# Kernel optimization log

Measured on AMD Instinct MI355X. Metric: run time of the kernel, lower is better.

The kernel has to match this reference:

```python
import jax, jax.numpy as jnp
import numpy as np
from jax import lax

B, C, T, K, L, G = 4, 256, 2048, 7, 2, 32


def _conv1d(x, w, b, pad=0, groups=1):
    # x: [B,C,T], w: [O, C//groups, kw]
    y = lax.conv_general_dilated(x, w, window_strides=(1,), padding=[(pad, pad)],
                                 dimension_numbers=("NCH", "OIH", "NCH"),
                                 feature_group_count=groups)
    return y + b[None, :, None]


def _conv2d(x, w, b, pad=(0, 0), groups=1):
    # x: [B,C,H,W], w: [O, C//groups, kh, kw]
    y = lax.conv_general_dilated(x, w, window_strides=(1, 1),
                                 padding=[(pad[0], pad[0]), (pad[1], pad[1])],
                                 dimension_numbers=("NCHW", "OIHW", "NCHW"),
                                 feature_group_count=groups)
    return y + b[None, :, None, None]


def _knn_dis(x, k):
    # x: [B,C,T] -> neighbor indices [B,T,k] by (negative) squared euclidean distance
    xx = jnp.sum(x * x, axis=1)                       # [B,T]
    inner = jnp.einsum("bcm,bcn->bmn", x, x)          # [B,T,T]
    pd = -xx[:, :, None] + 2.0 * inner - xx[:, None, :]  # -||x_m - x_n||^2
    _, idx = lax.top_k(pd, k)                          # nearest = largest of -dist^2
    return idx


def _graph_feature(x, idx):
    # x: [B,C,T], idx: [B,T,K] -> style=1 feature [B,2C,T,K] = cat(neighbor, center)
    xt = jnp.transpose(x, (0, 2, 1))                   # [B,T,C]
    bidx = jnp.arange(x.shape[0])[:, None, None]
    nb = xt[bidx, idx]                                 # [B,T,K,C] gather
    ctr = jnp.broadcast_to(xt[:, :, None, :], nb.shape)
    feat = jnp.concatenate([nb, ctr], axis=-1)         # [B,T,K,2C]
    return jnp.transpose(feat, (0, 3, 1, 2))           # [B,2C,T,K]


def setup_inputs() -> dict:
    key = jax.random.key(0)
    ks = jax.random.split(key, 9)
    s = 0.05
    return {
        "x": jax.random.normal(ks[0], (B, C, T), jnp.float32),
        "tw1": jax.random.normal(ks[1], (L, C, C, 1), jnp.float32) * s,
        "tb1": jax.random.normal(ks[2], (L, C), jnp.float32) * s,
        "tw2": jax.random.normal(ks[3], (L, C, C // G, 5), jnp.float32) * s,
        "tb2": jax.random.normal(ks[4], (L, C), jnp.float32) * s,
        "dw1": jax.random.normal(ks[5], (L, C, 2 * C, 1, 1), jnp.float32) * s,
        "db1": jax.random.normal(ks[6], (L, C), jnp.float32) * s,
        "dw2": jax.random.normal(ks[7], (L, C, C // G, 5, 5), jnp.float32) * s,
        "db2": jax.random.normal(ks[8], (L, C), jnp.float32) * s,
    }


def reference(x, tw1, tb1, tw2, tb2, dw1, db1, dw2, db2):
    for i in range(L):
        identity = x
        # temporal branch: 1x1 conv -> GELU -> grouped conv1d k=5 (pad=2)
        h = jax.nn.gelu(_conv1d(x, tw1[i], tb1[i]), approximate=False)
        tout = _conv1d(h, tw2[i], tb2[i], pad=2, groups=G)            # [B,C,T]
        # dynamic graph branch: euclidean knn -> gather -> DConv2D -> max over k
        idx = _knn_dis(x, K)                                           # [B,T,K]
        feat = _graph_feature(x, idx)                                  # [B,2C,T,K]
        g = jax.nn.gelu(_conv2d(feat, dw1[i], db1[i]), approximate=False)
        g = _conv2d(g, dw2[i], db2[i], pad=(2, 2), groups=G)          # [B,C,T,K]
        dout = jnp.max(g, axis=-1)                                     # [B,C,T]
        x = tout + dout + identity
    return x
```

## Files before the change

### kernel.cpp

```cpp
#include <hip/hip_runtime.h>
#include <math.h>

#define Bq 4
#define Cc 256
#define Tt 2048
#define Kk 7
#define NTOP 10
#define CG 8
#define Ll 2
#define NO 768

typedef __attribute__((ext_vector_type(8))) short short8;
typedef __attribute__((ext_vector_type(4))) float floatx4;
typedef __attribute__((ext_vector_type(2))) float floatx2;

__device__ __forceinline__ float gelu_f(float v) {
  return 0.5f * v * (1.0f + erff(v * 0.70710678118654752440f));
}

__device__ __forceinline__ float erf_fast(float x) {
  float ax = fabsf(x);
  float t = __builtin_amdgcn_rcpf(fmaf(0.3275911f, ax, 1.0f));
  float y = t * (0.254829592f + t * (-0.284496736f + t * (1.421413741f +
            t * (-1.453152027f + t * 1.061405429f))));
  float r = 1.0f - y * __expf(-ax * ax);
  return copysignf(r, x);
}
__device__ __forceinline__ float gelu_fast(float v) {
  return 0.5f * v * (1.0f + erf_fast(v * 0.70710678118654752440f));
}

__global__ void transpose_x(const float* __restrict__ x, float* __restrict__ xT,
                            unsigned short* __restrict__ xh,
                            unsigned short* __restrict__ xl) {
  __shared__ float tile[32][33];
  int b = blockIdx.z;
  int t0 = blockIdx.x * 32, c0 = blockIdx.y * 32;
  int tx = threadIdx.x, ty = threadIdx.y;
  const float* xb = x + (size_t)b * Cc * Tt;
  for (int r = ty; r < 32; r += 8)
    tile[r][tx] = xb[(size_t)(c0 + r) * Tt + t0 + tx];
  __syncthreads();
  size_t base = (size_t)b * Tt * Cc;
  for (int r = ty; r < 32; r += 8) {
    float v = tile[tx][r];
    size_t o = base + (size_t)(t0 + r) * Cc + c0 + tx;
    xT[o] = v;
    unsigned int u = __float_as_uint(v);
    unsigned short h = (unsigned short)((u + 0x7fffu + ((u >> 16) & 1u)) >> 16);
    float f = v - __uint_as_float((unsigned int)h << 16);
    unsigned int ul = __float_as_uint(f);
    xh[o] = h;
    xl[o] = (unsigned short)((ul + 0x7fffu + ((ul >> 16) & 1u)) >> 16);
  }
}

__global__ __launch_bounds__(512) void sqnorm_xt(
    const float* __restrict__ xT, float* __restrict__ xx) {
  int b = blockIdx.y;
  int t = blockIdx.x * 8 + (threadIdx.x >> 6);
  int lane = threadIdx.x & 63;
  const float* row = xT + ((size_t)b * Tt + t) * Cc;
  float4 v = *(const float4*)(row + lane * 4);
  float acc = v.x * v.x + v.y * v.y + v.z * v.z + v.w * v.w;
#pragma unroll
  for (int off = 1; off < 64; off <<= 1) acc += __shfl_xor(acc, off);
  if (lane == 0) xx[(size_t)b * Tt + t] = acc;
}

__global__ __launch_bounds__(256) void pw_conv8_all(
    const float* __restrict__ x, const float* __restrict__ tw1,
    const float* __restrict__ tb1, const float* __restrict__ dw1,
    const float* __restrict__ db1, float* __restrict__ hb,
    float* __restrict__ cb, float* __restrict__ nb) {
  int t = blockIdx.x * 256 + threadIdx.x;
  int oy = blockIdx.y;
  int b = blockIdx.z;
  int range = oy >> 5;
  int o0 = (oy & 31) * 8;
  const float* W; int wstride, woff; const float* bias; float* dst; int dg;
  if (range == 0)      { W = tw1; wstride = Cc;     woff = 0;  bias = tb1;     dst = hb; dg = 1; }
  else if (range == 1) { W = dw1; wstride = 2 * Cc; woff = Cc; bias = db1;     dst = cb; dg = 0; }
  else                 { W = dw1; wstride = 2 * Cc; woff = 0;  bias = nullptr; dst = nb; dg = 0; }
  const float* xp = x + (size_t)b * Cc * Tt + t;
  const float* wp = W + (size_t)o0 * wstride + woff;
  float acc[8];
#pragma unroll
  for (int j = 0; j < 8; ++j) acc[j] = bias ? bias[o0 + j] : 0.f;
  for (int c = 0; c < Cc; c += 4) {
    float xv0 = xp[(size_t)c * Tt];
    float xv1 = xp[(size_t)(c + 1) * Tt];
    float xv2 = xp[(size_t)(c + 2) * Tt];
    float xv3 = xp[(size_t)(c + 3) * Tt];
#pragma unroll
    for (int j = 0; j < 8; ++j) {
      const float* wr = wp + (size_t)j * wstride + c;
      float a = acc[j];
      a = fmaf(wr[0], xv0, a);
      a = fmaf(wr[1], xv1, a);
      a = fmaf(wr[2], xv2, a);
      a = fmaf(wr[3], xv3, a);
      acc[j] = a;
    }
  }
#pragma unroll
  for (int j = 0; j < 8; ++j) {
    float v = acc[j];
    if (dg) v = gelu_f(v);
    dst[((size_t)b * Cc + o0 + j) * Tt + t] = v;
  }
}

__global__ __launch_bounds__(256) void wsplit(
    const float* __restrict__ tw1, const float* __restrict__ dw1,
    unsigned short* __restrict__ wh, unsigned short* __restrict__ wl) {
  int o = blockIdx.x;
  int c = threadIdx.x;
  float v;
  if (o < 256) v = tw1[(size_t)o * Cc + c];
  else if (o < 512) v = dw1[(size_t)(o - 256) * (2 * Cc) + Cc + c];
  else v = dw1[(size_t)(o - 512) * (2 * Cc) + c];
  unsigned int u = __float_as_uint(v);
  unsigned short h = (unsigned short)((u + 0x7fffu + ((u >> 16) & 1u)) >> 16);
  float f = v - __uint_as_float((unsigned int)h << 16);
  unsigned int ul = __float_as_uint(f);
  wh[(size_t)o * Cc + c] = h;
  wl[(size_t)o * Cc + c] = (unsigned short)((ul + 0x7fffu + ((ul >> 16) & 1u)) >> 16);
}

__global__ __launch_bounds__(256) void pw_gemm(
    const unsigned short* __restrict__ wh, const unsigned short* __restrict__ wl,
    const unsigned short* __restrict__ xh, const unsigned short* __restrict__ xl,
    const float* __restrict__ tb1, const float* __restrict__ db1,
    float* __restrict__ hb, float* __restrict__ cb, float* __restrict__ nb) {
  __shared__ __align__(16) unsigned short Ah[128][40], Al[128][40];
  __shared__ __align__(16) unsigned short Bh[128][40], Bl[128][40];
  int mt = blockIdx.x;
  int b = mt >> 4;
  int t0 = (mt & 15) * 128;
  int o0 = blockIdx.y * 128;
  int tid = threadIdx.x;
  int w = tid >> 6, lane = tid & 63, quad = lane >> 4, l15 = lane & 15;
  int wm = (w >> 1) * 64, wn = (w & 1) * 64;
  floatx4 acc[4][4];
#pragma unroll
  for (int i = 0; i < 4; ++i)
#pragma unroll
    for (int j = 0; j < 4; ++j) acc[i][j] = (floatx4){0.f, 0.f, 0.f, 0.f};

  const unsigned short* xhb = xh + ((size_t)b * Tt + t0) * Cc;
  const unsigned short* xlb = xl + ((size_t)b * Tt + t0) * Cc;
  int sr = tid >> 1;
  int sq = (tid & 1) * 2;
  for (int kc = 0; kc < Cc; kc += 32) {
    __syncthreads();
    {
      const unsigned short* am = wh + (size_t)(o0 + sr) * Cc + kc + sq * 8;
      *(uint4*)&Ah[sr][sq * 8] = *(const uint4*)am;
      *(uint4*)&Ah[sr][sq * 8 + 8] = *(const uint4*)(am + 8);
      const unsigned short* al = wl + (size_t)(o0 + sr) * Cc + kc + sq * 8;
      *(uint4*)&Al[sr][sq * 8] = *(const uint4*)al;
      *(uint4*)&Al[sr][sq * 8 + 8] = *(const uint4*)(al + 8);
      const unsigned short* bm = xhb + (size_t)sr * Cc + kc + sq * 8;
      *(uint4*)&Bh[sr][sq * 8] = *(const uint4*)bm;
      *(uint4*)&Bh[sr][sq * 8 + 8] = *(const uint4*)(bm + 8);
      const unsigned short* bl = xlb + (size_t)sr * Cc + kc + sq * 8;
      *(uint4*)&Bl[sr][sq * 8] = *(const uint4*)bl;
      *(uint4*)&Bl[sr][sq * 8 + 8] = *(const uint4*)(bl + 8);
    }
    __syncthreads();
    int ka = quad * 8;
    short8 a_h[4], a_l[4], b_h[4], b_l[4];
#pragma unroll
    for (int f = 0; f < 4; ++f) {
      a_h[f] = *(const short8*)&Ah[wm + f * 16 + l15][ka];
      a_l[f] = *(const short8*)&Al[wm + f * 16 + l15][ka];
      b_h[f] = *(const short8*)&Bh[wn + f * 16 + l15][ka];
      b_l[f] = *(const short8*)&Bl[wn + f * 16 + l15][ka];
    }
#pragma unroll
    for (int fm = 0; fm < 4; ++fm)
#pragma unroll
      for (int fn = 0; fn < 4; ++fn) {
        acc[fm][fn] = __builtin_amdgcn_mfma_f32_16x16x32_bf16(a_h[fm], b_h[fn], acc[fm][fn], 0, 0, 0);
        acc[fm][fn] = __builtin_amdgcn_mfma_f32_16x16x32_bf16(a_h[fm], b_l[fn], acc[fm][fn], 0, 0, 0);
        acc[fm][fn] = __builtin_amdgcn_mfma_f32_16x16x32_bf16(a_l[fm], b_h[fn], acc[fm][fn], 0, 0, 0);
      }
  }
  int range = o0 >> 8;
  float* dst = (range == 0) ? hb : (range == 1) ? cb : nb;
  const float* bias = (range == 0) ? tb1 : (range == 1) ? db1 : nullptr;
  int ol0 = o0 & 255;
#pragma unroll
  for (int fm = 0; fm < 4; ++fm) {
    int o = ol0 + wm + fm * 16 + quad * 4;
#pragma unroll
    for (int r = 0; r < 4; ++r) {
      float bv = bias ? bias[o + r] : 0.f;
      size_t rowoff = ((size_t)b * Cc + o + r) * Tt + t0;
#pragma unroll
      for (int fn = 0; fn < 4; ++fn) {
        int t = wn + fn * 16 + l15;
        float v = acc[fm][fn][r] + bv;
        if (range == 0) v = gelu_f(v);
        dst[rowoff + t] = v;
      }
    }
  }
}

__global__ __launch_bounds__(256) void score_gemm(
    const unsigned short* __restrict__ xh, const unsigned short* __restrict__ xl,
    const float* __restrict__ xx, float* __restrict__ S, int bbase) {
  __shared__ __align__(16) unsigned short Ah[128][40], Al[128][40];
  __shared__ __align__(16) unsigned short Bh[128][40], Bl[128][40];
  int lb = blockIdx.z;
  int b = bbase + lb;
  int m0 = blockIdx.y * 128, n0 = blockIdx.x * 128;
  int tid = threadIdx.x;
  int w = tid >> 6, lane = tid & 63, quad = lane >> 4, l15 = lane & 15;
  int wm = (w >> 1) * 64, wn = (w & 1) * 64;
  const unsigned short* xhb = xh + (size_t)b * Tt * Cc;
  const unsigned short* xlb = xl + (size_t)b * Tt * Cc;
  const float* xxb = xx + (size_t)b * Tt;
  float* Sb = S + (size_t)lb * Tt * Tt;
  floatx4 acc[4][4];
#pragma unroll
  for (int i = 0; i < 4; ++i)
#pragma unroll
    for (int j = 0; j < 4; ++j) acc[i][j] = (floatx4){0.f, 0.f, 0.f, 0.f};

  int sr = tid >> 1;
  int sq = (tid & 1) * 2;
  for (int kc = 0; kc < Cc; kc += 32) {
    __syncthreads();
    {
      const unsigned short* am = xhb + (size_t)(m0 + sr) * Cc + kc + sq * 8;
      *(uint4*)&Ah[sr][sq * 8] = *(const uint4*)am;
      *(uint4*)&Ah[sr][sq * 8 + 8] = *(const uint4*)(am + 8);
      const unsigned short* al = xlb + (size_t)(m0 + sr) * Cc + kc + sq * 8;
      *(uint4*)&Al[sr][sq * 8] = *(const uint4*)al;
      *(uint4*)&Al[sr][sq * 8 + 8] = *(const uint4*)(al + 8);
      const unsigned short* bm = xhb + (size_t)(n0 + sr) * Cc + kc + sq * 8;
      *(uint4*)&Bh[sr][sq * 8] = *(const uint4*)bm;
      *(uint4*)&Bh[sr][sq * 8 + 8] = *(const uint4*)(bm + 8);
      const unsigned short* bl = xlb + (size_t)(n0 + sr) * Cc + kc + sq * 8;
      *(uint4*)&Bl[sr][sq * 8] = *(const uint4*)bl;
      *(uint4*)&Bl[sr][sq * 8 + 8] = *(const uint4*)(bl + 8);
    }
    __syncthreads();
    int ka = quad * 8;
    short8 a_h[4], a_l[4], b_h[4], b_l[4];
#pragma unroll
    for (int f = 0; f < 4; ++f) {
      a_h[f] = *(const short8*)&Ah[wm + f * 16 + l15][ka];
      a_l[f] = *(const short8*)&Al[wm + f * 16 + l15][ka];
      b_h[f] = *(const short8*)&Bh[wn + f * 16 + l15][ka];
      b_l[f] = *(const short8*)&Bl[wn + f * 16 + l15][ka];
    }
#pragma unroll
    for (int fm = 0; fm < 4; ++fm)
#pragma unroll
      for (int fn = 0; fn < 4; ++fn) {
        acc[fm][fn] = __builtin_amdgcn_mfma_f32_16x16x32_bf16(a_h[fm], b_h[fn], acc[fm][fn], 0, 0, 0);
        acc[fm][fn] = __builtin_amdgcn_mfma_f32_16x16x32_bf16(a_h[fm], b_l[fn], acc[fm][fn], 0, 0, 0);
        acc[fm][fn] = __builtin_amdgcn_mfma_f32_16x16x32_bf16(a_l[fm], b_h[fn], acc[fm][fn], 0, 0, 0);
      }
  }
#pragma unroll
  for (int fn = 0; fn < 4; ++fn) {
    int n = n0 + wn + fn * 16 + l15;
    float xv = xxb[n];
#pragma unroll
    for (int fm = 0; fm < 4; ++fm) {
      int m = m0 + wm + fm * 16 + quad * 4;
#pragma unroll
      for (int r = 0; r < 4; ++r)
        Sb[(size_t)(m + r) * Tt + n] = fmaf(2.f, acc[fm][fn][r], -xv);
    }
  }
}

__global__ __launch_bounds__(512) void topk_scan(
    const float* __restrict__ S, int* __restrict__ idx10, int bbase) {
  int lb = blockIdx.z;
  int m = blockIdx.x * 8 + (threadIdx.x >> 6);
  int lane = threadIdx.x & 63;
  const float* row = S + ((size_t)lb * Tt + m) * Tt;
  float s[NTOP]; int idl[NTOP];
#pragma unroll
  for (int j = 0; j < NTOP; ++j) { s[j] = -INFINITY; idl[j] = 0x7fffffff; }
  for (int c0 = lane * 4; c0 < Tt; c0 += 256) {
    float4 v = *(const float4*)(row + c0);
    float cand[4] = {v.x, v.y, v.z, v.w};
#pragma unroll
    for (int e = 0; e < 4; ++e) {
      float sc = cand[e];
      if (sc > s[NTOP - 1]) {
        s[NTOP - 1] = sc; idl[NTOP - 1] = c0 + e;
#pragma unroll
        for (int j = NTOP - 1; j > 0; --j) {
          if (s[j] > s[j - 1]) {
            float ts = s[j]; s[j] = s[j - 1]; s[j - 1] = ts;
            int ti = idl[j]; idl[j] = idl[j - 1]; idl[j - 1] = ti;
          }
        }
      }
    }
  }
  int ptr = 0;
  for (int r = 0; r < NTOP; ++r) {
    float cs = (ptr < NTOP) ? s[ptr] : -INFINITY;
    int cid = (ptr < NTOP) ? idl[ptr] : 0x7fffffff;
    float bs = cs; int bi = cid;
#pragma unroll
    for (int off = 1; off < 64; off <<= 1) {
      float os = __shfl_xor(bs, off);
      int oi = __shfl_xor(bi, off);
      if (os > bs || (os == bs && oi < bi)) { bs = os; bi = oi; }
    }
    if (cid == bi) ptr++;
    if (lane == 0) idx10[((size_t)(bbase + lb) * Tt + m) * NTOP + r] = bi;
  }
}

__global__ __launch_bounds__(64) void knn_rescore(
    const float* __restrict__ xT, const int* __restrict__ idx10,
    int* __restrict__ idxout) {
  int t = blockIdx.x;
  int b = blockIdx.y;
  int lane = threadIdx.x;
  const float* xTb = xT + (size_t)b * Tt * Cc;
  const float* xm = xTb + (size_t)t * Cc;
  double sc = -1e300;
  int cid = 0x7fffffff;
  if (lane < NTOP) {
    int j = idx10[((size_t)b * Tt + t) * NTOP + lane];
    const float* xn = xTb + (size_t)j * Cc;
    double dot = 0.0, nn = 0.0;
    for (int c = 0; c < Cc; c += 4) {
      float4 a = *(const float4*)(xm + c);
      float4 v = *(const float4*)(xn + c);
      dot += (double)a.x * v.x + (double)a.y * v.y + (double)a.z * v.z + (double)a.w * v.w;
      nn  += (double)v.x * v.x + (double)v.y * v.y + (double)v.z * v.z + (double)v.w * v.w;
    }
    sc = 2.0 * dot - nn;
    cid = j;
  }
  for (int r = 0; r < Kk; ++r) {
    double bs = sc; int bi = cid;
#pragma unroll
    for (int off = 1; off < 64; off <<= 1) {
      double os = __shfl_xor(bs, off);
      int oi = __shfl_xor(bi, off);
      if (os > bs || (os == bs && oi < bi)) { bs = os; bi = oi; }
    }
    if (cid == bi) { sc = -1e300; cid = 0x7fffffff; }
    if (lane == 0) idxout[((size_t)b * Tt + t) * Kk + r] = bi;
  }
}

template <int FAST>
__global__ __launch_bounds__(256) void graph_tail(
    const float* __restrict__ h, const float* __restrict__ ctr,
    const float* __restrict__ nbr, const int* __restrict__ idx,
    const float* __restrict__ tw2, const float* __restrict__ tb2,
    const float* __restrict__ dw2, const float* __restrict__ db2,
    const float* __restrict__ xin, float* __restrict__ xout) {
  __shared__ __align__(16) float gt[CG][Kk][68];
  __shared__ __align__(16) float ht[CG][68];
  __shared__ int jt[68][Kk];
  int t0 = blockIdx.x * 64;
  int g = blockIdx.y;
  int b = blockIdx.z;
  int tid = threadIdx.x;
  const float* hg   = h   + ((size_t)b * Cc + g * CG) * Tt;
  const float* ctrg = ctr + ((size_t)b * Cc + g * CG) * Tt;
  const float* nbrg = nbr + ((size_t)b * Cc + g * CG) * Tt;

  {
    const int* ib = idx + ((size_t)b * Tt + t0 - 2) * Kk;
    for (int e = tid; e < 68 * Kk; e += 256) {
      int tg = t0 - 2 + e / Kk;
      jt[e / Kk][e % Kk] = (tg >= 0 && tg < Tt) ? ib[e] : 0;
    }
    for (int e = tid; e < CG * 68; e += 256) {
      int ci = e / 68, tl = e % 68;
      int tg = t0 - 2 + tl;
      ht[ci][tl] = (tg >= 0 && tg < Tt) ? hg[(size_t)ci * Tt + tg] : 0.f;
    }
  }
  __syncthreads();
  for (int e = tid; e < CG * Kk * 68; e += 256) {
    int ci = e / (Kk * 68), rem = e % (Kk * 68), k = rem / 68, tl = rem % 68;
    int tg = t0 - 2 + tl;
    float v = 0.f;
    if (tg >= 0 && tg < Tt) {
      int j = jt[tl][k];
      float pre = ctrg[(size_t)ci * Tt + tg] + nbrg[(size_t)ci * Tt + j];
      v = FAST ? gelu_fast(pre) : gelu_f(pre);
    }
    gt[ci][k][tl] = v;
  }
  __syncthreads();

  int ol = tid >> 5, tl2 = (tid & 31) * 2;
  int o = g * CG + ol;

  const float* w2 = tw2 + (size_t)o * CG * 5;
  float bt = tb2[o];
  floatx2 acct = {bt, bt};
  for (int ci = 0; ci < CG; ++ci) {
    floatx2 p0 = *(const floatx2*)&ht[ci][tl2];
    floatx2 p1 = *(const floatx2*)&ht[ci][tl2 + 2];
    floatx2 p2 = *(const floatx2*)&ht[ci][tl2 + 4];
    float r6[6] = {p0.x, p0.y, p1.x, p1.y, p2.x, p2.y};
#pragma unroll
    for (int dt = 0; dt < 5; ++dt) {
      float wv = w2[ci * 5 + dt];
      floatx2 wv2 = {wv, wv};
      floatx2 rp = {r6[dt], r6[dt + 1]};
      acct = __builtin_elementwise_fma(wv2, rp, acct);
    }
  }

  const float* wp = dw2 + (size_t)o * CG * 25;
  float bv = db2[o];
  floatx2 acc[Kk];
#pragma unroll
  for (int k = 0; k < Kk; ++k) acc[k] = (floatx2){bv, bv};

  for (int ci = 0; ci < CG; ++ci) {
    float w[25];
#pragma unroll
    for (int i = 0; i < 25; ++i) w[i] = wp[ci * 25 + i];
#pragma unroll
    for (int kin = 0; kin < Kk; ++kin) {
      floatx2 p0 = *(const floatx2*)&gt[ci][kin][tl2];
      floatx2 p1 = *(const floatx2*)&gt[ci][kin][tl2 + 2];
      floatx2 p2 = *(const floatx2*)&gt[ci][kin][tl2 + 4];
      float r6[6] = {p0.x, p0.y, p1.x, p1.y, p2.x, p2.y};
      floatx2 rp[5];
#pragma unroll
      for (int dt = 0; dt < 5; ++dt) rp[dt] = (floatx2){r6[dt], r6[dt + 1]};
#pragma unroll
      for (int dk = 0; dk < 5; ++dk) {
        int k = kin + 2 - dk;
        if (k < 0 || k >= Kk) continue;
#pragma unroll
        for (int dt = 0; dt < 5; ++dt) {
          float wv = w[dt * 5 + dk];
          floatx2 wv2 = {wv, wv};
          acc[k] = __builtin_elementwise_fma(wv2, rp[dt], acc[k]);
        }
      }
    }
  }
  floatx2 m = acc[0];
#pragma unroll
  for (int k = 1; k < Kk; ++k) m = __builtin_elementwise_max(m, acc[k]);
  size_t off = ((size_t)b * Cc + o) * Tt + t0 + tl2;
  floatx2 xv = *(const floatx2*)&xin[off];
  floatx2 r;
  r.x = acct.x + m.x + xv.x;
  r.y = acct.y + m.y + xv.y;
  *(floatx2*)&xout[off] = r;
}

extern "C" void kernel_launch(void* const* d_in, const int* in_sizes, int n_in,
                              void* d_out, int out_size, void* d_ws, size_t ws_size,
                              hipStream_t stream) {
  const float* x0  = (const float*)d_in[0];
  const float* tw1 = (const float*)d_in[1];
  const float* tb1 = (const float*)d_in[2];
  const float* tw2 = (const float*)d_in[3];
  const float* tb2 = (const float*)d_in[4];
  const float* dw1 = (const float*)d_in[5];
  const float* db1 = (const float*)d_in[6];
  const float* dw2 = (const float*)d_in[7];
  const float* db2 = (const float*)d_in[8];
  float* out = (float*)d_out;

  float* ws = (float*)d_ws;
  const size_t NCT = (size_t)Bq * Cc * Tt;
  float* x1   = ws;
  float* hbuf = x1 + NCT;
  float* cbuf = hbuf + NCT;
  float* xT   = cbuf + NCT;
  unsigned short* xh = (unsigned short*)(xT + NCT);
  unsigned short* xl = xh + NCT;
  unsigned short* wh = xl + NCT;
  unsigned short* wl = wh + (size_t)NO * Cc;
  float* S    = (float*)(wl + (size_t)NO * Cc);
  float* xx   = S + 2 * (size_t)Tt * Tt;
  int* idxb   = (int*)(xx + (size_t)Bq * Tt);
  int* idx10  = idxb + (size_t)Bq * Tt * Kk;
  float* nbr  = xT;

  for (int i = 0; i < Ll; ++i) {
    const float* xin = (i == 0) ? x0 : x1;
    float* xout = (i == Ll - 1) ? out : x1;

    transpose_x<<<dim3(Tt/32, Cc/32, Bq), dim3(32, 8), 0, stream>>>(xin, xT, xh, xl);
    sqnorm_xt<<<dim3(Tt/8, Bq), 512, 0, stream>>>(xT, xx);
    for (int bp = 0; bp < Bq; bp += 2) {
      score_gemm<<<dim3(16, 16, 2), 256, 0, stream>>>(xh, xl, xx, S, bp);
      topk_scan<<<dim3(Tt/8, 1, 2), 512, 0, stream>>>(S, idx10, bp);
    }
    knn_rescore<<<dim3(Tt, Bq), 64, 0, stream>>>(xT, idx10, idxb);

    if (i == 0) {
      pw_conv8_all<<<dim3(Tt/256, 96, Bq), 256, 0, stream>>>(
          xin, tw1 + (size_t)i * Cc * Cc, tb1 + (size_t)i * Cc,
          dw1 + (size_t)i * Cc * 2 * Cc, db1 + (size_t)i * Cc,
          hbuf, cbuf, nbr);
      graph_tail<0><<<dim3(Tt/64, Cc/CG, Bq), 256, 0, stream>>>(
          hbuf, cbuf, nbr, idxb, tw2 + (size_t)i * Cc * CG * 5, tb2 + (size_t)i * Cc,
          dw2 + (size_t)i * Cc * CG * 25, db2 + (size_t)i * Cc, xin, xout);
    } else {
      wsplit<<<dim3(NO), 256, 0, stream>>>(
          tw1 + (size_t)i * Cc * Cc, dw1 + (size_t)i * Cc * 2 * Cc, wh, wl);
      pw_gemm<<<dim3(64, NO/128), 256, 0, stream>>>(
          wh, wl, xh, xl, tb1 + (size_t)i * Cc, db1 + (size_t)i * Cc,
          hbuf, cbuf, nbr);
      graph_tail<1><<<dim3(Tt/64, Cc/CG, Bq), 256, 0, stream>>>(
          hbuf, cbuf, nbr, idxb, tw2 + (size_t)i * Cc * CG * 5, tb2 + (size_t)i * Cc,
          dw2 + (size_t)i * Cc * CG * 25, db2 + (size_t)i * Cc, xin, xout);
    }
  }
}
```

Baseline: 595.2 us.

## Transpose neighbor projections to time-major for contiguous gathers in graph tail

Adds a transpose kernel that lays the neighbor projection buffer out as [B,T,C] so graph_tail can fetch all 8 group channels of a neighbor with two float4 loads. Before, each channel's neighbor value was a scattered scalar load. The center projection is also staged in shared memory, so each thread loops over channels in registers instead of reloading it per (channel,k). The cost is an extra transpose launch plus a full [B,T,C] write and read per layer, and more workspace.

```diff
diff --git a/kernel.cpp b/kernel.cpp
--- a/kernel.cpp
+++ b/kernel.cpp
@@ -55,6 +55,20 @@
   }
 }
 
+__global__ void transpose_f(const float* __restrict__ src, float* __restrict__ dst) {
+  __shared__ float tile[32][33];
+  int b = blockIdx.z;
+  int t0 = blockIdx.x * 32, c0 = blockIdx.y * 32;
+  int tx = threadIdx.x, ty = threadIdx.y;
+  const float* sb = src + (size_t)b * Cc * Tt;
+  for (int r = ty; r < 32; r += 8)
+    tile[r][tx] = sb[(size_t)(c0 + r) * Tt + t0 + tx];
+  __syncthreads();
+  float* db = dst + (size_t)b * Tt * Cc;
+  for (int r = ty; r < 32; r += 8)
+    db[(size_t)(t0 + r) * Cc + c0 + tx] = tile[tx][r];
+}
+
 __global__ __launch_bounds__(512) void sqnorm_xt(
     const float* __restrict__ xT, float* __restrict__ xx) {
   int b = blockIdx.y;
@@ -363,44 +377,53 @@
 template <int FAST>
 __global__ __launch_bounds__(256) void graph_tail(
     const float* __restrict__ h, const float* __restrict__ ctr,
-    const float* __restrict__ nbr, const int* __restrict__ idx,
+    const float* __restrict__ nbrT, const int* __restrict__ idx,
     const float* __restrict__ tw2, const float* __restrict__ tb2,
     const float* __restrict__ dw2, const float* __restrict__ db2,
     const float* __restrict__ xin, float* __restrict__ xout) {
   __shared__ __align__(16) float gt[CG][Kk][68];
   __shared__ __align__(16) float ht[CG][68];
-  __shared__ int jt[68][Kk];
+  __shared__ __align__(16) float ct[CG][68];
+  __shared__ int jt[Kk * 68];
   int t0 = blockIdx.x * 64;
   int g = blockIdx.y;
   int b = blockIdx.z;
   int tid = threadIdx.x;
   const float* hg   = h   + ((size_t)b * Cc + g * CG) * Tt;
   const float* ctrg = ctr + ((size_t)b * Cc + g * CG) * Tt;
-  const float* nbrg = nbr + ((size_t)b * Cc + g * CG) * Tt;
+  const float* nbT  = nbrT + (size_t)b * Tt * Cc + g * CG;
 
   {
     const int* ib = idx + ((size_t)b * Tt + t0 - 2) * Kk;
-    for (int e = tid; e < 68 * Kk; e += 256) {
-      int tg = t0 - 2 + e / Kk;
-      jt[e / Kk][e % Kk] = (tg >= 0 && tg < Tt) ? ib[e] : 0;
+    for (int p = tid; p < Kk * 68; p += 256) {
+      int k = p / 68, tl = p - k * 68;
+      int tg = t0 - 2 + tl;
+      jt[p] = (tg >= 0 && tg < Tt) ? ib[tl * Kk + k] : 0;
     }
     for (int e = tid; e < CG * 68; e += 256) {
-      int ci = e / 68, tl = e % 68;
+      int ci = e / 68, tl = e - ci * 68;
       int tg = t0 - 2 + tl;
-      ht[ci][tl] = (tg >= 0 && tg < Tt) ? hg[(size_t)ci * Tt + tg] : 0.f;
+      int valid = (tg >= 0 && tg < Tt);
+      ht[ci][tl] = valid ? hg[(size_t)ci * Tt + tg] : 0.f;
+      ct[ci][tl] = valid ? ctrg[(size_t)ci * Tt + tg] : 0.f;
     }
   }
   __syncthreads();
-  for (int e = tid; e < CG * Kk * 68; e += 256) {
-    int ci = e / (Kk * 68), rem = e % (Kk * 68), k = rem / 68, tl = rem % 68;
+  for (int p = tid; p < Kk * 68; p += 256) {
+    int k = p / 68, tl = p - k * 68;
     int tg = t0 - 2 + tl;
-    float v = 0.f;
-    if (tg >= 0 && tg < Tt) {
-      int j = jt[tl][k];
-      float pre = ctrg[(size_t)ci * Tt + tg] + nbrg[(size_t)ci * Tt + j];
-      v = FAST ? gelu_fast(pre) : gelu_f(pre);
-    }
-    gt[ci][k][tl] = v;
+    int valid = (tg >= 0 && tg < Tt);
+    int j = jt[p];
+    const float* np = nbT + (size_t)j * Cc;
+    float4 n0 = *(const float4*)np;
+    float4 n1 = *(const float4*)(np + 4);
+    float ch[8] = {n0.x, n0.y, n0.z, n0.w, n1.x, n1.y, n1.z, n1.w};
+#pragma unroll
+    for (int ci = 0; ci < CG; ++ci) {
+      float pre = ct[ci][tl] + ch[ci];
+      float v = FAST ? gelu_fast(pre) : gelu_f(pre);
+      gt[ci][k][tl] = valid ? v : 0.f;
+    }
   }
   __syncthreads();
 
@@ -495,6 +518,7 @@
   float* xx   = S + 2 * (size_t)Tt * Tt;
   int* idxb   = (int*)(xx + (size_t)Bq * Tt);
   int* idx10  = idxb + (size_t)Bq * Tt * Kk;
+  float* nbrT = (float*)(idx10 + (size_t)Bq * Tt * NTOP);
   float* nbr  = xT;
 
   for (int i = 0; i < Ll; ++i) {
@@ -514,17 +538,21 @@
           xin, tw1 + (size_t)i * Cc * Cc, tb1 + (size_t)i * Cc,
           dw1 + (size_t)i * Cc * 2 * Cc, db1 + (size_t)i * Cc,
           hbuf, cbuf, nbr);
-      graph_tail<0><<<dim3(Tt/64, Cc/CG, Bq), 256, 0, stream>>>(
-          hbuf, cbuf, nbr, idxb, tw2 + (size_t)i * Cc * CG * 5, tb2 + (size_t)i * Cc,
-          dw2 + (size_t)i * Cc * CG * 25, db2 + (size_t)i * Cc, xin, xout);
     } else {
       wsplit<<<dim3(NO), 256, 0, stream>>>(
           tw1 + (size_t)i * Cc * Cc, dw1 + (size_t)i * Cc * 2 * Cc, wh, wl);
       pw_gemm<<<dim3(64, NO/128), 256, 0, stream>>>(
           wh, wl, xh, xl, tb1 + (size_t)i * Cc, db1 + (size_t)i * Cc,
           hbuf, cbuf, nbr);
+    }
+    transpose_f<<<dim3(Tt/32, Cc/32, Bq), dim3(32, 8), 0, stream>>>(nbr, nbrT);
+    if (i == 0) {
+      graph_tail<0><<<dim3(Tt/64, Cc/CG, Bq), 256, 0, stream>>>(
+          hbuf, cbuf, nbrT, idxb, tw2 + (size_t)i * Cc * CG * 5, tb2 + (size_t)i * Cc,
+          dw2 + (size_t)i * Cc * CG * 25, db2 + (size_t)i * Cc, xin, xout);
+    } else {
       graph_tail<1><<<dim3(Tt/64, Cc/CG, Bq), 256, 0, stream>>>(
-          hbuf, cbuf, nbr, idxb, tw2 + (size_t)i * Cc * CG * 5, tb2 + (size_t)i * Cc,
+          hbuf, cbuf, nbrT, idxb, tw2 + (size_t)i * Cc * CG * 5, tb2 + (size_t)i * Cc,
           dw2 + (size_t)i * Cc * CG * 25, db2 + (size_t)i * Cc, xin, xout);
     }
   }
```

New measurement: 590.8 us. About the same (-0.7%).
